# Kernel tuning notes

Measured on AMD Instinct MI355X. Metric: run time of the kernel, lower is better.

Reference implementation:

```python
import jax, jax.numpy as jnp
import numpy as np

B, N, DIM, H, E = 2, 2048, 1024, 16, 8
HD = DIM // H
SCALE = HD ** -0.5


def setup_inputs() -> dict:
    key = jax.random.key(0)
    ks = jax.random.split(key, 6)
    s = DIM ** -0.5
    return {
        "x": jax.random.normal(ks[0], (B, N, DIM), dtype=jnp.float32),
        "w_qkv": jax.random.normal(ks[1], (3 * DIM, DIM), dtype=jnp.float32) * s,
        "b_qkv": jnp.zeros((3 * DIM,), dtype=jnp.float32),
        "w_proj": jax.random.normal(ks[2], (DIM, DIM), dtype=jnp.float32) * s,
        "b_proj": jnp.zeros((DIM,), dtype=jnp.float32),
        "rel_pos": jax.random.normal(ks[3], (1, H, E, E), dtype=jnp.float32),
    }


def reference(x, w_qkv, b_qkv, w_proj, b_proj, rel_pos):
    tpe = N // E  # tokens per entity (tile count)
    # qkv: [B,N,3*DIM] -> [3,B,H,N,HD]
    qkv = (jnp.einsum("bnc,dc->bnd", x, w_qkv) + b_qkv)
    qkv = qkv.reshape(B, N, 3, H, HD).transpose(2, 0, 3, 1, 4)
    q, k, v = qkv[0], qkv[1], qkv[2]
    attn = jnp.einsum("bhnd,bhmd->bhnm", q, k) * SCALE
    # torch .repeat tiles the ExE bias: bias[i,j] = rel_pos[i % E, j % E]
    rel_bias = jnp.tile(rel_pos, (B, 1, tpe, tpe))
    attn = jax.nn.softmax(attn + rel_bias, axis=-1)
    out = jnp.einsum("bhnm,bhmd->bhnd", attn, v)
    out = out.transpose(0, 2, 1, 3).reshape(B, N, DIM)
    return jnp.einsum("bnc,dc->bnd", out, w_proj) + b_proj
```

## Files before the change

kernel.cpp:

```cpp
#include <hip/hip_runtime.h>
#include <hip/hip_bf16.h>
#include <stdint.h>

#define B_ 2
#define N_ 2048
#define DIM_ 1024
#define H_ 16
#define HD_ 64
#define NT_ 32

typedef __attribute__((ext_vector_type(8))) short short8;
typedef __attribute__((ext_vector_type(4))) float f32x4;
typedef __attribute__((ext_vector_type(16))) float f32x16;

#define LOG2E_ 1.4426950408889634f
#define SBF_ (0.125f * LOG2E_)

__device__ __forceinline__ unsigned short f2bf(float f) {
  __bf16 h = (__bf16)f;
  return __builtin_bit_cast(unsigned short, h);
}

__device__ __forceinline__ void gload_lds16(const void* g, void* l) {
  __builtin_amdgcn_global_load_lds(
      (const __attribute__((address_space(1))) unsigned int*)g,
      (__attribute__((address_space(3))) unsigned int*)l,
      16, 0, 0);
}

#define XN4_ 1048576
#define WQ4_ 786432
__global__ __launch_bounds__(256) void cvt_all_kernel(
    const float4* __restrict__ x, const float4* __restrict__ wq,
    const float4* __restrict__ wp,
    ushort4* __restrict__ xb, ushort4* __restrict__ wqb, ushort4* __restrict__ wpb) {
  int i = blockIdx.x * 256 + threadIdx.x;
  const float4* src;
  ushort4* dst;
  if (i < XN4_) {
    src = x + i; dst = xb + i;
  } else if (i < XN4_ + WQ4_) {
    src = wq + (i - XN4_); dst = wqb + (i - XN4_);
  } else {
    src = wp + (i - XN4_ - WQ4_); dst = wpb + (i - XN4_ - WQ4_);
  }
  float4 v = *src;
  ushort4 o;
  o.x = f2bf(v.x); o.y = f2bf(v.y); o.z = f2bf(v.z); o.w = f2bf(v.w);
  *dst = o;
}

__device__ __forceinline__ void gemm128_mainloop(
    const ushort* __restrict__ A, const ushort* __restrict__ Bw, int K,
    int bm, int bn, ushort* As, ushort* Bs, f32x4 acc[4][4]) {
  const int tid = threadIdx.x;
  const int lane = tid & 63;
  const int w = tid >> 6, wr = w >> 1, wc = w & 1;
  const int fr = lane & 15, fq = lane >> 4;
  const int srow = tid >> 3, scol = (tid & 7) * 8;

  const ushort* Ag = A + (size_t)(bm * 128 + srow) * K + scol;
  const ushort* Bg = Bw + (size_t)(bn * 128 + srow) * K + scol;
  ushort* Asd = As + tid * 8;
  ushort* Bsd = Bs + tid * 8;

  for (int kt = 0; kt < K; kt += 64) {
    __syncthreads();
#pragma unroll
    for (int c = 0; c < 4; ++c) {
      gload_lds16(Ag + (size_t)(c * 32) * K + kt, Asd + c * 2048);
      gload_lds16(Bg + (size_t)(c * 32) * K + kt, Bsd + c * 2048);
    }
    __syncthreads();

    short8 af[2][4], bf[2][4];
#pragma unroll
    for (int kk = 0; kk < 2; ++kk) {
#pragma unroll
      for (int mi = 0; mi < 4; ++mi)
        af[kk][mi] = *(const short8*)&As[(wr * 64 + mi * 16 + fr) * 64 + kk * 32 + fq * 8];
#pragma unroll
      for (int ni = 0; ni < 4; ++ni)
        bf[kk][ni] = *(const short8*)&Bs[(wc * 64 + ni * 16 + fr) * 64 + kk * 32 + fq * 8];
    }
#pragma unroll
    for (int kk = 0; kk < 2; ++kk)
#pragma unroll
      for (int mi = 0; mi < 4; ++mi)
#pragma unroll
        for (int ni = 0; ni < 4; ++ni)
          acc[mi][ni] = __builtin_amdgcn_mfma_f32_16x16x32_bf16(
              bf[kk][ni], af[kk][mi], acc[mi][ni], 0, 0, 0);
  }
}

__global__ __launch_bounds__(256) void gemm_qkv_kernel(
    const ushort* __restrict__ xb, const ushort* __restrict__ wqkv,
    const float* __restrict__ bqkv,
    ushort* __restrict__ qo, ushort* __restrict__ ko, ushort* __restrict__ vo) {
  __shared__ ushort As[128 * 64];
  __shared__ ushort Bs[128 * 64];
  f32x4 acc[4][4] = {};
  const int bn = blockIdx.x, bm = blockIdx.y;
  gemm128_mainloop(xb, wqkv, DIM_, bm, bn, As, Bs, acc);

  const int tid = threadIdx.x, lane = tid & 63;
  const int w = tid >> 6, wr = w >> 1, wc = w & 1;
  const int fr = lane & 15, fq = lane >> 4;
#pragma unroll
  for (int mi = 0; mi < 4; ++mi) {
    int ng = bm * 128 + wr * 64 + mi * 16 + fr;
    int b = ng >> 11, n = ng & 2047;
#pragma unroll
    for (int ni = 0; ni < 4; ++ni) {
      int colb = bn * 128 + wc * 64 + ni * 16 + fq * 4;
      float4 b4 = *(const float4*)&bqkv[colb];
      int i3 = colb >> 10, h = (colb >> 6) & 15, hdq = colb & 63;
      float v0 = acc[mi][ni][0] + b4.x;
      float v1 = acc[mi][ni][1] + b4.y;
      float v2 = acc[mi][ni][2] + b4.z;
      float v3 = acc[mi][ni][3] + b4.w;
      if (i3 == 2) {
        size_t base = ((size_t)((b * H_ + h) * HD_ + hdq)) * N_ + n;
        vo[base]          = f2bf(v0);
        vo[base + N_]     = f2bf(v1);
        vo[base + 2 * N_] = f2bf(v2);
        vo[base + 3 * N_] = f2bf(v3);
      } else {
        const float s = (i3 == 0) ? SBF_ : 1.0f;
        ushort* base = (i3 == 0) ? qo : ko;
        ushort4 o;
        o.x = f2bf(v0 * s); o.y = f2bf(v1 * s);
        o.z = f2bf(v2 * s); o.w = f2bf(v3 * s);
        *(ushort4*)&base[((size_t)(b * H_ + h) * N_ + n) * HD_ + hdq] = o;
      }
    }
  }
}

__global__ __launch_bounds__(256) void gemm_proj_kernel(
    const ushort* __restrict__ ao, const ushort* __restrict__ wp,
    const float* __restrict__ bp, float* __restrict__ out) {
  __shared__ ushort As[128 * 64];
  __shared__ ushort Bs[128 * 64];
  f32x4 acc[4][4] = {};
  const int bn = blockIdx.x, bm = blockIdx.y;
  gemm128_mainloop(ao, wp, DIM_, bm, bn, As, Bs, acc);

  const int tid = threadIdx.x, lane = tid & 63;
  const int w = tid >> 6, wr = w >> 1, wc = w & 1;
  const int fr = lane & 15, fq = lane >> 4;
#pragma unroll
  for (int mi = 0; mi < 4; ++mi) {
    int mg = bm * 128 + wr * 64 + mi * 16 + fr;
#pragma unroll
    for (int ni = 0; ni < 4; ++ni) {
      int colb = bn * 128 + wc * 64 + ni * 16 + fq * 4;
      float4 b4 = *(const float4*)&bp[colb];
      float4 o;
      o.x = acc[mi][ni][0] + b4.x;
      o.y = acc[mi][ni][1] + b4.y;
      o.z = acc[mi][ni][2] + b4.z;
      o.w = acc[mi][ni][3] + b4.w;
      *(float4*)&out[(size_t)mg * DIM_ + colb] = o;
    }
  }
}

__global__ __launch_bounds__(256, 2) void attn_kernel(
    const ushort* __restrict__ Qg, const ushort* __restrict__ Kg,
    const ushort* __restrict__ Vtg, const float* __restrict__ rel,
    ushort* __restrict__ outb) {
  __shared__ ushort Ks[2][64 * 64];
  __shared__ ushort Vs[2][64 * 64];

  const int bid = blockIdx.x;
  const int xcd = bid & 7, idx = bid >> 3;
  const int bh = xcd * 4 + (idx >> 4);
  const int q0 = (idx & 15) * 128;
  const int h = bh & 15;
  const int tid = threadIdx.x, lane = tid & 63, w = tid >> 6;
  const int ql = lane & 31, hi = lane >> 5;

  f32x16 biasC;
  {
    float b0 = rel[h * 64 + (ql & 7) * 8 + 0 + 4 * hi] * LOG2E_;
    float b1 = rel[h * 64 + (ql & 7) * 8 + 1 + 4 * hi] * LOG2E_;
    float b2 = rel[h * 64 + (ql & 7) * 8 + 2 + 4 * hi] * LOG2E_;
    float b3 = rel[h * 64 + (ql & 7) * 8 + 3 + 4 * hi] * LOG2E_;
#pragma unroll
    for (int z = 0; z < 16; z += 4) {
      biasC[z] = b0; biasC[z + 1] = b1; biasC[z + 2] = b2; biasC[z + 3] = b3;
    }
  }

  const ushort* qrow = Qg + ((size_t)bh * N_ + q0 + w * 32 + ql) * HD_;
  short8 qf[4];
#pragma unroll
  for (int kk = 0; kk < 4; ++kk)
    qf[kk] = *(const short8*)&qrow[kk * 16 + hi * 8];

  float l = 0.f;
  f32x16 oacc[2] = {};
  f32x16 sA[2], sB[2];

  const int srow = tid >> 3, scol = (tid & 7) * 8;
  const int swsrc = scol ^ ((srow & 7) << 3);
  int kcol[4];
#pragma unroll
  for (int kk = 0; kk < 4; ++kk)
    kcol[kk] = (kk * 16 + hi * 8) ^ ((ql & 7) << 3);

#define STAGE_K(t, bb)                                                              \
  {                                                                                 \
    const size_t kv0 = (size_t)(t) * 64;                                            \
    _Pragma("unroll") for (int c = 0; c < 2; ++c)                                   \
        gload_lds16(Kg + ((size_t)bh * N_ + kv0 + c * 32 + srow) * HD_ + swsrc,     \
                    &Ks[bb][c * 2048 + tid * 8]);                                   \
  }
#define STAGE_V(t, bb)                                                              \
  {                                                                                 \
    const size_t kv0 = (size_t)(t) * 64;                                            \
    _Pragma("unroll") for (int c = 0; c < 2; ++c)                                   \
        gload_lds16(Vtg + ((size_t)(bh * HD_ + c * 32 + srow)) * N_ + kv0 + swsrc,  \
                    &Vs[bb][c * 2048 + tid * 8]);                                   \
  }

#define QKT(S, K_)                                                                  \
  {                                                                                 \
    S[0] = biasC;                                                                   \
    S[1] = biasC;                                                                   \
    __builtin_amdgcn_s_setprio(1);                                                  \
    _Pragma("unroll") for (int kk = 0; kk < 4; ++kk) {                              \
      short8 kf0 = *(const short8*)&(K_)[ql * 64 + kcol[kk]];                       \
      short8 kf1 = *(const short8*)&(K_)[(32 + ql) * 64 + kcol[kk]];                \
      S[0] = __builtin_amdgcn_mfma_f32_32x32x16_bf16(kf0, qf[kk], S[0], 0, 0, 0);   \
      S[1] = __builtin_amdgcn_mfma_f32_32x32x16_bf16(kf1, qf[kk], S[1], 0, 0, 0);   \
    }                                                                               \
    __builtin_amdgcn_s_setprio(0);                                                  \
  }

#define SOFTPV(S, V_)                                                               \
  {                                                                                 \
    float rs_[4] = {0.f, 0.f, 0.f, 0.f};                                            \
    uint32_t c[2][8];                                                               \
    _Pragma("unroll") for (int blk = 0; blk < 2; ++blk) {                           \
      _Pragma("unroll") for (int i = 0; i < 8; ++i) {                               \
        float pa = __builtin_amdgcn_exp2f(S[blk][2 * i]);                           \
        float pb = __builtin_amdgcn_exp2f(S[blk][2 * i + 1]);                       \
        rs_[i & 3] += pa + pb;                                                      \
        c[blk][i] = ((uint32_t)f2bf(pb) << 16) | f2bf(pa);                          \
      }                                                                             \
    }                                                                               \
    float rs = (rs_[0] + rs_[1]) + (rs_[2] + rs_[3]);                               \
    rs += __shfl_xor(rs, 32, 64);                                                   \
    l += rs;                                                                        \
    _Pragma("unroll") for (int blk = 0; blk < 2; ++blk) {                           \
      asm("v_permlane32_swap_b32 %0, %1" : "+v"(c[blk][0]), "+v"(c[blk][2]));       \
      asm("v_permlane32_swap_b32 %0, %1" : "+v"(c[blk][1]), "+v"(c[blk][3]));       \
      asm("v_permlane32_swap_b32 %0, %1" : "+v"(c[blk][4]), "+v"(c[blk][6]));       \
      asm("v_permlane32_swap_b32 %0, %1" : "+v"(c[blk][5]), "+v"(c[blk][7]));       \
    }                                                                               \
    __builtin_amdgcn_s_setprio(1);                                                  \
    _Pragma("unroll") for (int kk = 0; kk < 4; ++kk) {                              \
      union { uint32_t u[4]; short8 s8; } pb_;                                      \
      pb_.u[0] = c[kk >> 1][(kk & 1) * 4 + 0];                                      \
      pb_.u[1] = c[kk >> 1][(kk & 1) * 4 + 1];                                      \
      pb_.u[2] = c[kk >> 1][(kk & 1) * 4 + 2];                                      \
      pb_.u[3] = c[kk >> 1][(kk & 1) * 4 + 3];                                      \
      _Pragma("unroll") for (int db = 0; db < 2; ++db) {                            \
        short8 vf = *(const short8*)&(V_)[(db * 32 + ql) * 64 + kcol[kk]];          \
        oacc[db] = __builtin_amdgcn_mfma_f32_32x32x16_bf16(vf, pb_.s8, oacc[db], 0, 0, 0); \
      }                                                                             \
    }                                                                               \
    __builtin_amdgcn_s_setprio(0);                                                  \
  }

  STAGE_K(0, 0);
  STAGE_V(0, 0);
  __syncthreads();
  QKT(sA, Ks[0]);
  STAGE_K(1, 1);
  __syncthreads();

#pragma unroll 1
  for (int tt = 0; tt < 15; ++tt) {
    const int t = 2 * tt;
    STAGE_K(t + 2, 0);
    STAGE_V(t + 1, 1);
    QKT(sB, Ks[1]);
    SOFTPV(sA, Vs[0]);
    __syncthreads();
    STAGE_K(t + 3, 1);
    STAGE_V(t + 2, 0);
    QKT(sA, Ks[0]);
    SOFTPV(sB, Vs[1]);
    __syncthreads();
  }
  STAGE_V(31, 1);
  QKT(sB, Ks[1]);
  SOFTPV(sA, Vs[0]);
  __syncthreads();
  SOFTPV(sB, Vs[1]);

  const int b = bh >> 4;
  const float invl = 1.0f / l;
  const size_t rowbase = ((size_t)(b * N_ + q0 + w * 32 + ql)) * DIM_ + h * HD_;
#pragma unroll
  for (int db = 0; db < 2; ++db)
#pragma unroll
    for (int g = 0; g < 4; ++g) {
      ushort4 o;
      o.x = f2bf(oacc[db][4 * g + 0] * invl);
      o.y = f2bf(oacc[db][4 * g + 1] * invl);
      o.z = f2bf(oacc[db][4 * g + 2] * invl);
      o.w = f2bf(oacc[db][4 * g + 3] * invl);
      *(ushort4*)&outb[rowbase + db * 32 + 8 * g + 4 * hi] = o;
    }
#undef STAGE_K
#undef STAGE_V
#undef QKT
#undef SOFTPV
}

extern "C" void kernel_launch(void* const* d_in, const int* in_sizes, int n_in,
                              void* d_out, int out_size, void* d_ws, size_t ws_size,
                              hipStream_t stream) {
  const float* x      = (const float*)d_in[0];
  const float* w_qkv  = (const float*)d_in[1];
  const float* b_qkv  = (const float*)d_in[2];
  const float* w_proj = (const float*)d_in[3];
  const float* b_proj = (const float*)d_in[4];
  const float* rel    = (const float*)d_in[5];

  char* ws = (char*)d_ws;
  ushort* xb     = (ushort*)(ws + 0);
  ushort* wqkvb  = (ushort*)(ws + 8388608);
  ushort* wprojb = (ushort*)(ws + 14680064);
  ushort* qb     = (ushort*)(ws + 16777216);
  ushort* kb     = (ushort*)(ws + 25165824);
  ushort* vb     = (ushort*)(ws + 33554432);
  ushort* aob    = (ushort*)(ws + 41943040);
  (void)in_sizes; (void)n_in; (void)out_size; (void)ws_size;

  cvt_all_kernel<<<8192, 256, 0, stream>>>(
      (const float4*)x, (const float4*)w_qkv, (const float4*)w_proj,
      (ushort4*)xb, (ushort4*)wqkvb, (ushort4*)wprojb);

  gemm_qkv_kernel<<<dim3(24, 32), 256, 0, stream>>>(xb, wqkvb, b_qkv, qb, kb, vb);
  attn_kernel<<<512, 256, 0, stream>>>(qb, kb, vb, rel, aob);
  gemm_proj_kernel<<<dim3(8, 32), 256, 0, stream>>>(aob, wprojb, b_proj, (float*)d_out);
}
```

Measured before the change: 135.1 us.

## Split attention KV range across wave pairs and load V directly to registers

The attention kernel now gives each block 64 queries instead of 128 and splits the 2048 keys into two halves handled by two wave pairs. The partial outputs and row sums are combined through LDS at the end. V fragments are read straight from global memory into registers rather than staged through LDS. The grid doubles to 1024 blocks and occupancy is raised to 3 blocks per CU, aiming for more parallelism and less LDS traffic. In exchange, each K/V tile is reused by fewer queries, V global loads are uncached and uncoalesced, and a final cross-wave reduction is added.

```diff
diff --git a/kernel.cpp b/kernel.cpp
--- a/kernel.cpp
+++ b/kernel.cpp
@@ -7,7 +7,6 @@
 #define DIM_ 1024
 #define H_ 16
 #define HD_ 64
-#define NT_ 32
 
 typedef __attribute__((ext_vector_type(8))) short short8;
 typedef __attribute__((ext_vector_type(4))) float f32x4;
@@ -167,20 +166,21 @@
   }
 }
 
-__global__ __launch_bounds__(256, 2) void attn_kernel(
+__global__ __launch_bounds__(256, 3) void attn_kernel(
     const ushort* __restrict__ Qg, const ushort* __restrict__ Kg,
     const ushort* __restrict__ Vtg, const float* __restrict__ rel,
     ushort* __restrict__ outb) {
-  __shared__ ushort Ks[2][64 * 64];
-  __shared__ ushort Vs[2][64 * 64];
+  __shared__ alignas(16) unsigned char smem[32768];
+  ushort* KsB = (ushort*)smem;
 
   const int bid = blockIdx.x;
   const int xcd = bid & 7, idx = bid >> 3;
-  const int bh = xcd * 4 + (idx >> 4);
-  const int q0 = (idx & 15) * 128;
+  const int bh = xcd * 4 + (idx >> 5);
+  const int q0 = (idx & 31) * 64;
   const int h = bh & 15;
   const int tid = threadIdx.x, lane = tid & 63, w = tid >> 6;
   const int ql = lane & 31, hi = lane >> 5;
+  const int qg = w & 1, half = w >> 1;
 
   f32x16 biasC;
   {
@@ -194,18 +194,19 @@
     }
   }
 
-  const ushort* qrow = Qg + ((size_t)bh * N_ + q0 + w * 32 + ql) * HD_;
+  const ushort* qrow = Qg + ((size_t)bh * N_ + q0 + qg * 32 + ql) * HD_;
   short8 qf[4];
 #pragma unroll
   for (int kk = 0; kk < 4; ++kk)
     qf[kk] = *(const short8*)&qrow[kk * 16 + hi * 8];
 
+  const ushort* Vb0 = Vtg + ((size_t)(bh * HD_ + ql)) * N_;
+  const ushort* Vb1 = Vtg + ((size_t)(bh * HD_ + 32 + ql)) * N_;
+
   float l = 0.f;
   f32x16 oacc[2] = {};
-  f32x16 sA[2], sB[2];
-
-  const int srow = tid >> 3, scol = (tid & 7) * 8;
-  const int swsrc = scol ^ ((srow & 7) << 3);
+  f32x16 S[2];
+
   int kcol[4];
 #pragma unroll
   for (int kk = 0; kk < 4; ++kk)
@@ -213,114 +214,116 @@
 
 #define STAGE_K(t, bb)                                                              \
   {                                                                                 \
-    const size_t kv0 = (size_t)(t) * 64;                                            \
-    _Pragma("unroll") for (int c = 0; c < 2; ++c)                                   \
-        gload_lds16(Kg + ((size_t)bh * N_ + kv0 + c * 32 + srow) * HD_ + swsrc,     \
-                    &Ks[bb][c * 2048 + tid * 8]);                                   \
-  }
-#define STAGE_V(t, bb)                                                              \
-  {                                                                                 \
-    const size_t kv0 = (size_t)(t) * 64;                                            \
-    _Pragma("unroll") for (int c = 0; c < 2; ++c)                                   \
-        gload_lds16(Vtg + ((size_t)(bh * HD_ + c * 32 + srow)) * N_ + kv0 + swsrc,  \
-                    &Vs[bb][c * 2048 + tid * 8]);                                   \
-  }
-
-#define QKT(S, K_)                                                                  \
-  {                                                                                 \
-    S[0] = biasC;                                                                   \
-    S[1] = biasC;                                                                   \
-    __builtin_amdgcn_s_setprio(1);                                                  \
-    _Pragma("unroll") for (int kk = 0; kk < 4; ++kk) {                              \
-      short8 kf0 = *(const short8*)&(K_)[ql * 64 + kcol[kk]];                       \
-      short8 kf1 = *(const short8*)&(K_)[(32 + ql) * 64 + kcol[kk]];                \
-      S[0] = __builtin_amdgcn_mfma_f32_32x32x16_bf16(kf0, qf[kk], S[0], 0, 0, 0);   \
-      S[1] = __builtin_amdgcn_mfma_f32_32x32x16_bf16(kf1, qf[kk], S[1], 0, 0, 0);   \
-    }                                                                               \
-    __builtin_amdgcn_s_setprio(0);                                                  \
-  }
-
-#define SOFTPV(S, V_)                                                               \
-  {                                                                                 \
-    float rs_[4] = {0.f, 0.f, 0.f, 0.f};                                            \
-    uint32_t c[2][8];                                                               \
-    _Pragma("unroll") for (int blk = 0; blk < 2; ++blk) {                           \
-      _Pragma("unroll") for (int i = 0; i < 8; ++i) {                               \
-        float pa = __builtin_amdgcn_exp2f(S[blk][2 * i]);                           \
-        float pb = __builtin_amdgcn_exp2f(S[blk][2 * i + 1]);                       \
-        rs_[i & 3] += pa + pb;                                                      \
-        c[blk][i] = ((uint32_t)f2bf(pb) << 16) | f2bf(pa);                          \
-      }                                                                             \
-    }                                                                               \
-    float rs = (rs_[0] + rs_[1]) + (rs_[2] + rs_[3]);                               \
-    rs += __shfl_xor(rs, 32, 64);                                                   \
-    l += rs;                                                                        \
-    _Pragma("unroll") for (int blk = 0; blk < 2; ++blk) {                           \
-      asm("v_permlane32_swap_b32 %0, %1" : "+v"(c[blk][0]), "+v"(c[blk][2]));       \
-      asm("v_permlane32_swap_b32 %0, %1" : "+v"(c[blk][1]), "+v"(c[blk][3]));       \
-      asm("v_permlane32_swap_b32 %0, %1" : "+v"(c[blk][4]), "+v"(c[blk][6]));       \
-      asm("v_permlane32_swap_b32 %0, %1" : "+v"(c[blk][5]), "+v"(c[blk][7]));       \
-    }                                                                               \
-    __builtin_amdgcn_s_setprio(1);                                                  \
-    _Pragma("unroll") for (int kk = 0; kk < 4; ++kk) {                              \
-      union { uint32_t u[4]; short8 s8; } pb_;                                      \
-      pb_.u[0] = c[kk >> 1][(kk & 1) * 4 + 0];                                      \
-      pb_.u[1] = c[kk >> 1][(kk & 1) * 4 + 1];                                      \
-      pb_.u[2] = c[kk >> 1][(kk & 1) * 4 + 2];                                      \
-      pb_.u[3] = c[kk >> 1][(kk & 1) * 4 + 3];                                      \
-      _Pragma("unroll") for (int db = 0; db < 2; ++db) {                            \
-        short8 vf = *(const short8*)&(V_)[(db * 32 + ql) * 64 + kcol[kk]];          \
-        oacc[db] = __builtin_amdgcn_mfma_f32_32x32x16_bf16(vf, pb_.s8, oacc[db], 0, 0, 0); \
-      }                                                                             \
-    }                                                                               \
-    __builtin_amdgcn_s_setprio(0);                                                  \
+    const int hf = tid >> 7, r = tid & 127;                                         \
+    const size_t krow = (size_t)bh * N_ + (size_t)(hf * 16 + (t)) * 64;             \
+    _Pragma("unroll") for (int c = 0; c < 4; ++c)                                   \
+        gload_lds16(Kg + (krow + c * 16 + (r >> 3)) * HD_ +                         \
+                        (((r & 7) * 8) ^ (((r >> 3) & 7) << 3)),                    \
+                    &KsB[(hf * 2 + (bb)) * 4096 + c * 1024 + r * 8]);               \
   }
 
   STAGE_K(0, 0);
-  STAGE_V(0, 0);
   __syncthreads();
-  QKT(sA, Ks[0]);
-  STAGE_K(1, 1);
+
+#pragma unroll 2
+  for (int t = 0; t < 16; ++t) {
+    const int cur = t & 1;
+    const int kv0 = (half * 16 + t) * 64;
+
+    short8 vf[4][2];
+#pragma unroll
+    for (int kk = 0; kk < 4; ++kk) {
+      vf[kk][0] = *(const short8*)&Vb0[kv0 + kk * 16 + hi * 8];
+      vf[kk][1] = *(const short8*)&Vb1[kv0 + kk * 16 + hi * 8];
+    }
+
+    if (t < 15) STAGE_K(t + 1, cur ^ 1);
+
+    const ushort* K_ = KsB + (half * 2 + cur) * 4096;
+    S[0] = biasC;
+    S[1] = biasC;
+    __builtin_amdgcn_s_setprio(1);
+#pragma unroll
+    for (int kk = 0; kk < 4; ++kk) {
+      short8 kf0 = *(const short8*)&K_[ql * 64 + kcol[kk]];
+      short8 kf1 = *(const short8*)&K_[(32 + ql) * 64 + kcol[kk]];
+      S[0] = __builtin_amdgcn_mfma_f32_32x32x16_bf16(kf0, qf[kk], S[0], 0, 0, 0);
+      S[1] = __builtin_amdgcn_mfma_f32_32x32x16_bf16(kf1, qf[kk], S[1], 0, 0, 0);
+    }
+    __builtin_amdgcn_s_setprio(0);
+
+    float rs_[4] = {0.f, 0.f, 0.f, 0.f};
+    uint32_t c[2][8];
+#pragma unroll
+    for (int blk = 0; blk < 2; ++blk) {
+#pragma unroll
+      for (int i = 0; i < 8; ++i) {
+        float pa = __builtin_amdgcn_exp2f(S[blk][2 * i]);
+        float pb = __builtin_amdgcn_exp2f(S[blk][2 * i + 1]);
+        rs_[i & 3] += pa + pb;
+        c[blk][i] = ((uint32_t)f2bf(pb) << 16) | f2bf(pa);
+      }
+    }
+    float rs = (rs_[0] + rs_[1]) + (rs_[2] + rs_[3]);
+    rs += __shfl_xor(rs, 32, 64);
+    l += rs;
+#pragma unroll
+    for (int blk = 0; blk < 2; ++blk) {
+      asm("v_permlane32_swap_b32 %0, %1" : "+v"(c[blk][0]), "+v"(c[blk][2]));
+      asm("v_permlane32_swap_b32 %0, %1" : "+v"(c[blk][1]), "+v"(c[blk][3]));
+      asm("v_permlane32_swap_b32 %0, %1" : "+v"(c[blk][4]), "+v"(c[blk][6]));
+      asm("v_permlane32_swap_b32 %0, %1" : "+v"(c[blk][5]), "+v"(c[blk][7]));
+    }
+
+    __builtin_amdgcn_s_setprio(1);
+#pragma unroll
+    for (int kk = 0; kk < 4; ++kk) {
+      union { uint32_t u[4]; short8 s8; } pb_;
+      pb_.u[0] = c[kk >> 1][(kk & 1) * 4 + 0];
+      pb_.u[1] = c[kk >> 1][(kk & 1) * 4 + 1];
+      pb_.u[2] = c[kk >> 1][(kk & 1) * 4 + 2];
+      pb_.u[3] = c[kk >> 1][(kk & 1) * 4 + 3];
+      oacc[0] = __builtin_amdgcn_mfma_f32_32x32x16_bf16(vf[kk][0], pb_.s8, oacc[0], 0, 0, 0);
+      oacc[1] = __builtin_amdgcn_mfma_f32_32x32x16_bf16(vf[kk][1], pb_.s8, oacc[1], 0, 0, 0);
+    }
+    __builtin_amdgcn_s_setprio(0);
+    __syncthreads();
+  }
+#undef STAGE_K
+
+  float* Olds = (float*)smem;
+  float* Llds = (float*)(smem + 16384);
+  if (half == 1) {
+#pragma unroll
+    for (int db = 0; db < 2; ++db)
+#pragma unroll
+      for (int g = 0; g < 4; ++g) {
+        f32x4 v;
+        v[0] = oacc[db][4 * g + 0]; v[1] = oacc[db][4 * g + 1];
+        v[2] = oacc[db][4 * g + 2]; v[3] = oacc[db][4 * g + 3];
+        *(f32x4*)&Olds[(qg * 32 + ql) * 64 + db * 32 + 8 * g + 4 * hi] = v;
+      }
+    Llds[qg * 32 + ql] = l;
+  }
   __syncthreads();
-
-#pragma unroll 1
-  for (int tt = 0; tt < 15; ++tt) {
-    const int t = 2 * tt;
-    STAGE_K(t + 2, 0);
-    STAGE_V(t + 1, 1);
-    QKT(sB, Ks[1]);
-    SOFTPV(sA, Vs[0]);
-    __syncthreads();
-    STAGE_K(t + 3, 1);
-    STAGE_V(t + 2, 0);
-    QKT(sA, Ks[0]);
-    SOFTPV(sB, Vs[1]);
-    __syncthreads();
-  }
-  STAGE_V(31, 1);
-  QKT(sB, Ks[1]);
-  SOFTPV(sA, Vs[0]);
-  __syncthreads();
-  SOFTPV(sB, Vs[1]);
-
-  const int b = bh >> 4;
-  const float invl = 1.0f / l;
-  const size_t rowbase = ((size_t)(b * N_ + q0 + w * 32 + ql)) * DIM_ + h * HD_;
-#pragma unroll
-  for (int db = 0; db < 2; ++db)
-#pragma unroll
-    for (int g = 0; g < 4; ++g) {
-      ushort4 o;
-      o.x = f2bf(oacc[db][4 * g + 0] * invl);
-      o.y = f2bf(oacc[db][4 * g + 1] * invl);
-      o.z = f2bf(oacc[db][4 * g + 2] * invl);
-      o.w = f2bf(oacc[db][4 * g + 3] * invl);
-      *(ushort4*)&outb[rowbase + db * 32 + 8 * g + 4 * hi] = o;
-    }
-#undef STAGE_K
-#undef STAGE_V
-#undef QKT
-#undef SOFTPV
+  if (half == 0) {
+    const int b = bh >> 4;
+    float l2 = Llds[qg * 32 + ql];
+    float invl = 1.0f / (l + l2);
+    size_t rowbase = ((size_t)(b * N_ + q0 + qg * 32 + ql)) * DIM_ + h * HD_;
+#pragma unroll
+    for (int db = 0; db < 2; ++db)
+#pragma unroll
+      for (int g = 0; g < 4; ++g) {
+        f32x4 v = *(const f32x4*)&Olds[(qg * 32 + ql) * 64 + db * 32 + 8 * g + 4 * hi];
+        ushort4 o;
+        o.x = f2bf((oacc[db][4 * g + 0] + v[0]) * invl);
+        o.y = f2bf((oacc[db][4 * g + 1] + v[1]) * invl);
+        o.z = f2bf((oacc[db][4 * g + 2] + v[2]) * invl);
+        o.w = f2bf((oacc[db][4 * g + 3] + v[3]) * invl);
+        *(ushort4*)&outb[rowbase + db * 32 + 8 * g + 4 * hi] = o;
+      }
+  }
 }
 
 extern "C" void kernel_launch(void* const* d_in, const int* in_sizes, int n_in,
@@ -348,6 +351,6 @@
       (ushort4*)xb, (ushort4*)wqkvb, (ushort4*)wprojb);
 
   gemm_qkv_kernel<<<dim3(24, 32), 256, 0, stream>>>(xb, wqkvb, b_qkv, qb, kb, vb);
-  attn_kernel<<<512, 256, 0, stream>>>(qb, kb, vb, rel, aob);
+  attn_kernel<<<1024, 256, 0, stream>>>(qb, kb, vb, rel, aob);
   gemm_proj_kernel<<<dim3(8, 32), 256, 0, stream>>>(aob, wprojb, b_proj, (float*)d_out);
 }
```

New measurement: 161.9 us. 19.8% more time.

## Swizzle GEMM blocks per XCD and deepen attention K/V pipeline to four stages

Applied to the files above, without the earlier changes.

The QKV and projection GEMMs now launch a 1D grid and remap block IDs so that consecutive blocks on the same XCD cover neighbouring output tiles, aiming for better L2 reuse. The attention kernel grows its K/V shared-memory ring from two to four tiles and processes two tiles per half-iteration, staging the next pair while computing the current pair. This halves the number of barriers but doubles LDS use to 64KB per block, which may lower occupancy under launch_bounds(256,2). The QK^T of the next tile no longer overlaps the current softmax, which changes how the work is scheduled.

```diff
diff --git a/kernel.cpp b/kernel.cpp
--- a/kernel.cpp
+++ b/kernel.cpp
@@ -101,7 +101,9 @@
   __shared__ ushort As[128 * 64];
   __shared__ ushort Bs[128 * 64];
   f32x4 acc[4][4] = {};
-  const int bn = blockIdx.x, bm = blockIdx.y;
+  const int bid = blockIdx.x;
+  const int virt = (bid & 7) * 96 + (bid >> 3);
+  const int bm = virt / 24, bn = virt % 24;
   gemm128_mainloop(xb, wqkv, DIM_, bm, bn, As, Bs, acc);
 
   const int tid = threadIdx.x, lane = tid & 63;
@@ -144,7 +146,9 @@
   __shared__ ushort As[128 * 64];
   __shared__ ushort Bs[128 * 64];
   f32x4 acc[4][4] = {};
-  const int bn = blockIdx.x, bm = blockIdx.y;
+  const int bid = blockIdx.x;
+  const int virt = (bid & 7) * 32 + (bid >> 3);
+  const int bm = virt >> 3, bn = virt & 7;
   gemm128_mainloop(ao, wp, DIM_, bm, bn, As, Bs, acc);
 
   const int tid = threadIdx.x, lane = tid & 63;
@@ -171,8 +175,8 @@
     const ushort* __restrict__ Qg, const ushort* __restrict__ Kg,
     const ushort* __restrict__ Vtg, const float* __restrict__ rel,
     ushort* __restrict__ outb) {
-  __shared__ ushort Ks[2][64 * 64];
-  __shared__ ushort Vs[2][64 * 64];
+  __shared__ ushort Ks[4][4096];
+  __shared__ ushort Vs[4][4096];
 
   const int bid = blockIdx.x;
   const int xcd = bid & 7, idx = bid >> 3;
@@ -276,32 +280,30 @@
     __builtin_amdgcn_s_setprio(0);                                                  \
   }
 
-  STAGE_K(0, 0);
-  STAGE_V(0, 0);
+  STAGE_K(0, 0); STAGE_V(0, 0);
+  STAGE_K(1, 1); STAGE_V(1, 1);
   __syncthreads();
-  QKT(sA, Ks[0]);
-  STAGE_K(1, 1);
-  __syncthreads();
 
 #pragma unroll 1
-  for (int tt = 0; tt < 15; ++tt) {
-    const int t = 2 * tt;
-    STAGE_K(t + 2, 0);
-    STAGE_V(t + 1, 1);
+  for (int tt = 0; tt < 8; ++tt) {
+    const int t0 = 4 * tt;
+    STAGE_K(t0 + 2, 2); STAGE_V(t0 + 2, 2);
+    STAGE_K(t0 + 3, 3); STAGE_V(t0 + 3, 3);
+    QKT(sA, Ks[0]);
     QKT(sB, Ks[1]);
     SOFTPV(sA, Vs[0]);
-    __syncthreads();
-    STAGE_K(t + 3, 1);
-    STAGE_V(t + 2, 0);
-    QKT(sA, Ks[0]);
     SOFTPV(sB, Vs[1]);
     __syncthreads();
-  }
-  STAGE_V(31, 1);
-  QKT(sB, Ks[1]);
-  SOFTPV(sA, Vs[0]);
-  __syncthreads();
-  SOFTPV(sB, Vs[1]);
+    if (tt < 7) {
+      STAGE_K(t0 + 4, 0); STAGE_V(t0 + 4, 0);
+      STAGE_K(t0 + 5, 1); STAGE_V(t0 + 5, 1);
+    }
+    QKT(sA, Ks[2]);
+    QKT(sB, Ks[3]);
+    SOFTPV(sA, Vs[2]);
+    SOFTPV(sB, Vs[3]);
+    __syncthreads();
+  }
 
   const int b = bh >> 4;
   const float invl = 1.0f / l;
@@ -347,7 +349,7 @@
       (const float4*)x, (const float4*)w_qkv, (const float4*)w_proj,
       (ushort4*)xb, (ushort4*)wqkvb, (ushort4*)wprojb);
 
-  gemm_qkv_kernel<<<dim3(24, 32), 256, 0, stream>>>(xb, wqkvb, b_qkv, qb, kb, vb);
+  gemm_qkv_kernel<<<768, 256, 0, stream>>>(xb, wqkvb, b_qkv, qb, kb, vb);
   attn_kernel<<<512, 256, 0, stream>>>(qb, kb, vb, rel, aob);
-  gemm_proj_kernel<<<dim3(8, 32), 256, 0, stream>>>(aob, wprojb, b_proj, (float*)d_out);
-}
+  gemm_proj_kernel<<<256, 256, 0, stream>>>(aob, wprojb, b_proj, (float*)d_out);
+}
```

After: 136.3 us. About the same (+0.9%).
